# Kernel tuning notes

Hardware: AMD Instinct MI355X
Metric: run time of the kernel (lower is better)

The kernel has to match this reference:

```python
import jax, jax.numpy as jnp
import numpy as np

EPS = 1e-5  # BatchNorm eps (torch default)

def setup_inputs() -> dict:
    key = jax.random.key(0)
    ks = jax.random.split(key, 12)
    B, C, H, W = 4, 256, 64, 64
    IC = 128  # inter_channels = C // 2
    s = 1.0 / np.sqrt(C)
    si = 1.0 / np.sqrt(IC)
    return {
        "x": jax.random.normal(ks[0], (B, C, H, W), jnp.float32),
        "y": jax.random.normal(ks[1], (B, C, H, W), jnp.float32),
        "g_w": jax.random.normal(ks[2], (IC, C), jnp.float32) * s,
        "g_b": jax.random.normal(ks[3], (IC,), jnp.float32) * 0.01,
        "dx_w": jax.random.normal(ks[4], (IC, C), jnp.float32) * s,
        "dx_b": jax.random.normal(ks[5], (IC,), jnp.float32) * 0.01,
        "dy_w": jax.random.normal(ks[6], (IC, C), jnp.float32) * s,
        "dy_b": jax.random.normal(ks[7], (IC,), jnp.float32) * 0.01,
        "w_w": jax.random.normal(ks[8], (C, IC), jnp.float32) * si,
        "w_b": jax.random.normal(ks[9], (C,), jnp.float32) * 0.01,
        "bn_gamma": jax.random.normal(ks[10], (C,), jnp.float32),
        "bn_beta": jax.random.normal(ks[11], (C,), jnp.float32) * 0.01,
    }

def _conv1x1(t, w, b):
    # t: [B,C,H,W], w: [O,C], b: [O] -> [B,O,H,W]
    return jnp.einsum('bchw,oc->bohw', t, w) + b[None, :, None, None]

def reference(x, y, g_w, g_b, dx_w, dx_b, dy_w, dy_b, w_w, w_b, bn_gamma, bn_beta):
    B, C, H, W = x.shape
    IC = g_w.shape[0]
    N = H * W
    g_y = _conv1x1(y, g_w, g_b).reshape(B, IC, N).transpose(0, 2, 1)      # [B,N,IC]
    theta_x = _conv1x1(x, dx_w, dx_b).reshape(B, IC, N).transpose(0, 2, 1)  # [B,N,IC]
    phi_y = _conv1x1(y, dy_w, dy_b).reshape(B, IC, N)                      # [B,IC,N]
    f = jnp.einsum('bnc,bcm->bnm', theta_x, phi_y)                         # [B,N,N]
    f_div_C = jax.nn.softmax(f, axis=-1)
    y2 = jnp.einsum('bnm,bmc->bnc', f_div_C, g_y)                          # [B,N,IC]
    y2 = y2.transpose(0, 2, 1).reshape(B, IC, H, W)
    wy = _conv1x1(y2, w_w, w_b)                                            # [B,C,H,W]
    # BatchNorm2d in training mode: batch stats over (B,H,W) per channel
    mean = jnp.mean(wy, axis=(0, 2, 3), keepdims=True)
    var = jnp.var(wy, axis=(0, 2, 3), keepdims=True)
    wy_bn = (wy - mean) / jnp.sqrt(var + EPS)
    wy_bn = wy_bn * bn_gamma[None, :, None, None] + bn_beta[None, :, None, None]
    return wy_bn + x
```

## Files before the change

### kernel.cpp

```cpp
#include <hip/hip_runtime.h>
#include <hip/hip_bf16.h>
#include <math.h>

typedef unsigned short ushort_t;
typedef __attribute__((ext_vector_type(8))) short     short8;
typedef __attribute__((ext_vector_type(8))) _Float16  half8;
typedef __attribute__((ext_vector_type(8))) unsigned short ushort8;
typedef __attribute__((ext_vector_type(4))) float     float4v;

__device__ __forceinline__ float b2f(ushort_t u) {
    return __uint_as_float(((unsigned)u) << 16);
}
__device__ __forceinline__ ushort_t f2b(float f) {
    unsigned i = __float_as_uint(f);
    return (ushort_t)((i + 0x7FFFu + ((i >> 16) & 1u)) >> 16);
}
__device__ __forceinline__ void split2(float v, ushort_t& h, ushort_t& l) {
    h = f2b(v);
    l = f2b(v - b2f(h));
}
__device__ __forceinline__ void glds16(const ushort_t* g, ushort_t* l) {
    __builtin_amdgcn_global_load_lds((const __attribute__((address_space(1))) void*)g,
                                     (__attribute__((address_space(3))) void*)l, 16, 0, 0);
}

#define WTFH_OFF   0
#define WTFL_OFF   196608
#define WWBH_OFF   393216
#define WWBL_OFF   458752
#define BIAS_OFF   524288
#define STATS_OFF  526336
#define PROJF_OFF  1048576
#define GT_OFF     9437184
#define OPART_OFF  13631488
#define WY_OFF     1048576

__global__ void prep_k(const float* __restrict__ dx_w, const float* __restrict__ dy_w,
                       const float* __restrict__ g_w,  const float* __restrict__ dx_b,
                       const float* __restrict__ dy_b, const float* __restrict__ g_b,
                       const float* __restrict__ w_w,
                       ushort_t* __restrict__ wtfh, ushort_t* __restrict__ wtfl,
                       ushort_t* __restrict__ wwbh, ushort_t* __restrict__ wwbl,
                       float* __restrict__ bias) {
    int idx = blockIdx.x * 256 + threadIdx.x;
    int j = idx & 7, lane = (idx >> 3) & 63, kk = (idx >> 9) & 7, ot = idx >> 12;
    int o = ot * 16 + (lane & 15);
    int c = kk * 32 + ((lane >> 4) * 8) + j;
    float v;
    if (o < 128)      v = dx_w[o * 256 + c];
    else if (o < 256) v = dy_w[(o - 128) * 256 + c];
    else              v = g_w[(o - 256) * 256 + c];
    ushort_t h, l;
    split2(v, h, l);
    wtfh[idx] = h; wtfl[idx] = l;
    if (idx < 32768) {
        split2(w_w[idx], h, l);
        wwbh[idx] = h; wwbl[idx] = l;
    }
    if (idx < 384) {
        bias[idx] = (idx < 128) ? dx_b[idx]
                  : (idx < 256) ? dy_b[idx - 128]
                                : g_b[idx - 256];
    }
}

__global__ __launch_bounds__(256) void proj_k(const float* __restrict__ x,
                                              const float* __restrict__ y,
                                              const ushort_t* __restrict__ wtfh,
                                              const ushort_t* __restrict__ wtfl,
                                              const float* __restrict__ bias,
                                              ushort_t* __restrict__ projf,
                                              ushort_t* __restrict__ gT) {
    __shared__ ushort_t xT[2][32 * 256];
    int b = blockIdx.y, n0 = blockIdx.x * 32;
    int tid = threadIdx.x;
    int w = tid >> 6, lane = tid & 63;
    int mrow = lane & 15, quad = lane >> 4, koff = quad * 8;
    int half = w & 1, sect = w >> 1;
    int arow = half * 16 + mrow;

    for (int s = 0; s < 2; s++) {
        if (s) __syncthreads();
        const float* src = s ? y : x;
        #pragma unroll
        for (int i = 0; i < 4; i++) {
            int ch = tid + i * 256;
            int c = ch >> 2, off = (ch & 3) * 8;
            const float* p = src + (size_t)(b * 256 + c) * 4096 + n0 + off;
            float4v v0 = *(const float4v*)p;
            float4v v1 = *(const float4v*)(p + 4);
            #pragma unroll
            for (int jj = 0; jj < 4; jj++) {
                ushort_t h, l;
                split2(v0[jj], h, l);
                xT[0][(off + jj) * 256 + c] = h;
                xT[1][(off + jj) * 256 + c] = l;
                split2(v1[jj], h, l);
                xT[0][(off + 4 + jj) * 256 + c] = h;
                xT[1][(off + 4 + jj) * 256 + c] = l;
            }
        }
        __syncthreads();

        short8 fh[8], fl[8];
        #pragma unroll
        for (int kk = 0; kk < 8; kk++) {
            fh[kk] = *(const short8*)&xT[0][arow * 256 + kk * 32 + koff];
            fl[kk] = *(const short8*)&xT[1][arow * 256 + kk * 32 + koff];
        }

        int ot0 = s ? (8 + sect * 8) : (sect * 4);
        int ot1 = s ? (ot0 + 8) : (ot0 + 4);
        for (int ot = ot0; ot < ot1; ot++) {
            float4v acc = {0.f, 0.f, 0.f, 0.f};
            #pragma unroll
            for (int kk = 0; kk < 8; kk++) {
                short8 bh = *(const short8*)(wtfh + (size_t)((ot * 8 + kk) * 64 + lane) * 8);
                short8 bl = *(const short8*)(wtfl + (size_t)((ot * 8 + kk) * 64 + lane) * 8);
                acc = __builtin_amdgcn_mfma_f32_16x16x32_bf16(fh[kk], bh, acc, 0, 0, 0);
                acc = __builtin_amdgcn_mfma_f32_16x16x32_bf16(fh[kk], bl, acc, 0, 0, 0);
                acc = __builtin_amdgcn_mfma_f32_16x16x32_bf16(fl[kk], bh, acc, 0, 0, 0);
            }
            int o = ot * 16 + mrow;
            float bo = bias[o];
            #pragma unroll
            for (int r = 0; r < 4; r++) {
                int n = n0 + half * 16 + quad * 4 + r;
                float v = acc[r] + bo;
                if (ot < 16) {
                    _Float16 hf = (_Float16)v;
                    projf[(size_t)(b * 4096 + n) * 256 + o] = *(ushort_t*)&hf;
                } else {
                    gT[(size_t)(b * 128 + (o - 256)) * 4096 + n] = f2b(v);
                }
            }
        }
    }
}

__global__ __launch_bounds__(512, 2) void flash_k(const ushort_t* __restrict__ projf,
                                                  const ushort_t* __restrict__ gT,
                                                  float* __restrict__ opart,
                                                  float* __restrict__ oml,
                                                  int kqlog) {
    __shared__ __align__(16) ushort_t KsF[2][8192];
    __shared__ __align__(16) ushort_t VsF[2][8192];
    __shared__ __align__(16) ushort_t Ps[256 * 72];

    int b = blockIdx.y;
    int kq = blockIdx.x & ((1 << kqlog) - 1);
    int q0 = (blockIdx.x >> kqlog) * 256;
    int iters = 64 >> kqlog;
    int kt0 = kq * iters;
    int tid = threadIdx.x, w = tid >> 6, lane = tid & 63;
    int mrow = lane & 15, quad = lane >> 4, koff = quad * 8;

    int kRow[2], kCol[2], vIc[2], vOf[2], dstB[2];
    #pragma unroll
    for (int i = 0; i < 2; i++) {
        int ck = tid + i * 512, combo = ck >> 6, l2 = ck & 63;
        kRow[i] = (combo >> 2) * 16 + (l2 & 15);
        kCol[i] = 128 + (combo & 3) * 32 + (l2 >> 4) * 8;
        vIc[i]  = (combo >> 1) * 16 + (l2 & 15);
        vOf[i]  = (combo & 1) * 32 + (l2 >> 4) * 8;
        dstB[i] = (i * 512 + w * 64) * 8;
    }

    half8 qf[2][4];
    #pragma unroll
    for (int s = 0; s < 2; s++)
        #pragma unroll
        for (int kk = 0; kk < 4; kk++)
            qf[s][kk] = *(const half8*)(projf + (size_t)(b * 4096 + q0 + w * 32 + s * 16 + mrow) * 256
                                        + kk * 32 + koff);

    float4v oacc[2][8], oaccL[2];
    #pragma unroll
    for (int s = 0; s < 2; s++) {
        oaccL[s] = (float4v){0.f, 0.f, 0.f, 0.f};
        #pragma unroll
        for (int ot = 0; ot < 8; ot++) oacc[s][ot] = (float4v){0.f, 0.f, 0.f, 0.f};
    }
    short8 vones;
    #pragma unroll
    for (int j = 0; j < 8; j++) vones[j] = (short)0x3F80;

    {
        int kb = kt0 * 64;
        #pragma unroll
        for (int i = 0; i < 2; i++) {
            glds16(projf + (size_t)(b * 4096 + kb + kRow[i]) * 256 + kCol[i], &KsF[0][dstB[i]]);
            glds16(gT + (size_t)(b * 128 + vIc[i]) * 4096 + kb + vOf[i], &VsF[0][dstB[i]]);
        }
    }

    for (int kt = kt0; kt < kt0 + iters; kt++) {
        int cur = (kt - kt0) & 1;
        __syncthreads();
        if (kt + 1 < kt0 + iters) {
            int kb = (kt + 1) * 64;
            #pragma unroll
            for (int i = 0; i < 2; i++) {
                glds16(projf + (size_t)(b * 4096 + kb + kRow[i]) * 256 + kCol[i], &KsF[1 - cur][dstB[i]]);
                glds16(gT + (size_t)(b * 128 + vIc[i]) * 4096 + kb + vOf[i], &VsF[1 - cur][dstB[i]]);
            }
        }

        float4v sacc[2][4];
        #pragma unroll
        for (int ct = 0; ct < 4; ct++) {
            float4v a0 = {0.f, 0.f, 0.f, 0.f}, a1 = {0.f, 0.f, 0.f, 0.f};
            #pragma unroll
            for (int kk = 0; kk < 4; kk++) {
                half8 bh = *(const half8*)&KsF[cur][((ct * 4 + kk) * 64 + lane) * 8];
                a0 = __builtin_amdgcn_mfma_f32_16x16x32_f16(qf[0][kk], bh, a0, 0, 0, 0);
                a1 = __builtin_amdgcn_mfma_f32_16x16x32_f16(qf[1][kk], bh, a1, 0, 0, 0);
            }
            sacc[0][ct] = a0; sacc[1][ct] = a1;
        }

        #pragma unroll
        for (int s = 0; s < 2; s++)
            #pragma unroll
            for (int r = 0; r < 4; r++) {
                int prow = w * 32 + s * 16 + quad * 4 + r;
                #pragma unroll
                for (int ct = 0; ct < 4; ct++) {
                    float p = __builtin_exp2f(fmaf(sacc[s][ct][r], 1.44269504f, -92.332481f));
                    Ps[prow * 72 + ct * 16 + mrow] = f2b(p);
                }
            }
        __builtin_amdgcn_s_waitcnt(0xC07F);

        #pragma unroll
        for (int k2 = 0; k2 < 2; k2++) {
            short8 a0 = *(const short8*)&Ps[(w * 32 + mrow) * 72 + k2 * 32 + koff];
            short8 a1 = *(const short8*)&Ps[(w * 32 + 16 + mrow) * 72 + k2 * 32 + koff];
            #pragma unroll
            for (int ot = 0; ot < 8; ot++) {
                short8 bfr = *(const short8*)&VsF[cur][((ot * 2 + k2) * 64 + lane) * 8];
                oacc[0][ot] = __builtin_amdgcn_mfma_f32_16x16x32_bf16(a0, bfr, oacc[0][ot], 0, 0, 0);
                oacc[1][ot] = __builtin_amdgcn_mfma_f32_16x16x32_bf16(a1, bfr, oacc[1][ot], 0, 0, 0);
            }
            oaccL[0] = __builtin_amdgcn_mfma_f32_16x16x32_bf16(a0, vones, oaccL[0], 0, 0, 0);
            oaccL[1] = __builtin_amdgcn_mfma_f32_16x16x32_bf16(a1, vones, oaccL[1], 0, 0, 0);
        }
    }

    #pragma unroll
    for (int s = 0; s < 2; s++)
        #pragma unroll
        for (int ot = 0; ot < 8; ot++)
            #pragma unroll
            for (int r = 0; r < 4; r++) {
                int R = b * 4096 + q0 + w * 32 + s * 16 + quad * 4 + r;
                opart[((size_t)kq * 16384 + R) * 128 + ot * 16 + mrow] = oacc[s][ot][r];
            }
    if (mrow == 0) {
        #pragma unroll
        for (int s = 0; s < 2; s++)
            #pragma unroll
            for (int r = 0; r < 4; r++) {
                int R = b * 4096 + q0 + w * 32 + s * 16 + quad * 4 + r;
                oml[kq * 16384 + R] = oaccL[s][r];
            }
    }
}

__global__ __launch_bounds__(256) void wy_k(const float* __restrict__ opart,
                                            const float* __restrict__ oml,
                                            const ushort_t* __restrict__ wwbh,
                                            const ushort_t* __restrict__ wwbl,
                                            const float* __restrict__ w_b,
                                            ushort_t* __restrict__ wy, int KQ) {
    int b = blockIdx.y, n0 = blockIdx.x * 32;
    int tid = threadIdx.x, w = tid >> 6, lane = tid & 63;
    int mrow = lane & 15, quad = lane >> 4, koff = quad * 8;
    int half = w & 1, sect = w >> 1;
    int Rn = b * 4096 + n0 + half * 16 + mrow;

    float L = 0.f;
    for (int kq = 0; kq < KQ; kq++) L += oml[kq * 16384 + Rn];
    float invL = 1.f / L;

    short8 bfh[4], bfl[4];
    #pragma unroll
    for (int kk = 0; kk < 4; kk++) {
        float a[8];
        #pragma unroll
        for (int j = 0; j < 8; j++) a[j] = 0.f;
        for (int kq = 0; kq < KQ; kq++) {
            const float* p = opart + ((size_t)kq * 16384 + Rn) * 128 + kk * 32 + koff;
            float4v v0 = *(const float4v*)p;
            float4v v1 = *(const float4v*)(p + 4);
            #pragma unroll
            for (int j = 0; j < 4; j++) { a[j] += v0[j]; a[4 + j] += v1[j]; }
        }
        #pragma unroll
        for (int j = 0; j < 8; j++) {
            ushort_t h, l;
            split2(a[j] * invL, h, l);
            bfh[kk][j] = (short)h; bfl[kk][j] = (short)l;
        }
    }

    int coln = n0 + half * 16 + mrow;
    for (int cot = sect * 8; cot < sect * 8 + 8; cot++) {
        float4v acc = {0.f, 0.f, 0.f, 0.f};
        #pragma unroll
        for (int kk = 0; kk < 4; kk++) {
            size_t woff = (size_t)(cot * 16 + mrow) * 128 + kk * 32 + koff;
            short8 ah = *(const short8*)(wwbh + woff);
            short8 al = *(const short8*)(wwbl + woff);
            acc = __builtin_amdgcn_mfma_f32_16x16x32_bf16(ah, bfh[kk], acc, 0, 0, 0);
            acc = __builtin_amdgcn_mfma_f32_16x16x32_bf16(ah, bfl[kk], acc, 0, 0, 0);
            acc = __builtin_amdgcn_mfma_f32_16x16x32_bf16(al, bfh[kk], acc, 0, 0, 0);
        }
        #pragma unroll
        for (int r = 0; r < 4; r++) {
            int co = cot * 16 + quad * 4 + r;
            wy[(size_t)(b * 256 + co) * 4096 + coln] = f2b(acc[r] + w_b[co]);
        }
    }
}

__global__ __launch_bounds__(256) void stats_k(const ushort_t* __restrict__ wy,
                                               float* __restrict__ stats) {
    __shared__ float red[8];
    int co = blockIdx.x, tid = threadIdx.x, w = tid >> 6, lane = tid & 63;
    float s = 0.f, s2 = 0.f;
    #pragma unroll
    for (int i = 0; i < 8; i++) {
        int ch = tid + i * 256;
        int b = ch >> 9, n = (ch & 511) * 8;
        ushort8 v = *(const ushort8*)(wy + (size_t)(b * 256 + co) * 4096 + n);
        #pragma unroll
        for (int j = 0; j < 8; j++) { float f = b2f(v[j]); s += f; s2 += f * f; }
    }
    #pragma unroll
    for (int d = 1; d < 64; d <<= 1) { s += __shfl_xor(s, d, 64); s2 += __shfl_xor(s2, d, 64); }
    if (lane == 0) { red[w] = s; red[4 + w] = s2; }
    __syncthreads();
    if (tid == 0) {
        stats[co]       = red[0] + red[1] + red[2] + red[3];
        stats[256 + co] = red[4] + red[5] + red[6] + red[7];
    }
}

__global__ __launch_bounds__(256) void bn_k(const ushort_t* __restrict__ wy,
                                            const float* __restrict__ x,
                                            const float* __restrict__ gamma,
                                            const float* __restrict__ beta,
                                            const float* __restrict__ stats,
                                            float* __restrict__ out) {
    int idx = (blockIdx.x * 256 + threadIdx.x) * 8;
    int c = (idx >> 12) & 255;
    const float inv_cnt = 1.f / 16384.f;
    float mean = stats[c] * inv_cnt;
    float var  = stats[256 + c] * inv_cnt - mean * mean;
    float inv  = rsqrtf(var + 1e-5f);
    float scale = gamma[c] * inv;
    float shift = beta[c] - mean * scale;
    ushort8 wv = *(const ushort8*)(wy + idx);
    float4v x0 = *(const float4v*)(x + idx);
    float4v x1 = *(const float4v*)(x + idx + 4);
    float4v o0, o1;
    #pragma unroll
    for (int j = 0; j < 4; j++) {
        o0[j] = b2f(wv[j]) * scale + shift + x0[j];
        o1[j] = b2f(wv[4 + j]) * scale + shift + x1[j];
    }
    *(float4v*)(out + idx) = o0;
    *(float4v*)(out + idx + 4) = o1;
}

extern "C" void kernel_launch(void* const* d_in, const int* in_sizes, int n_in,
                              void* d_out, int out_size, void* d_ws, size_t ws_size,
                              hipStream_t stream) {
    const float* x    = (const float*)d_in[0];
    const float* y    = (const float*)d_in[1];
    const float* g_w  = (const float*)d_in[2];
    const float* g_b  = (const float*)d_in[3];
    const float* dx_w = (const float*)d_in[4];
    const float* dx_b = (const float*)d_in[5];
    const float* dy_w = (const float*)d_in[6];
    const float* dy_b = (const float*)d_in[7];
    const float* w_w  = (const float*)d_in[8];
    const float* w_b  = (const float*)d_in[9];
    const float* bn_g = (const float*)d_in[10];
    const float* bn_b = (const float*)d_in[11];

    char* ws = (char*)d_ws;
    ushort_t* wtfh  = (ushort_t*)(ws + WTFH_OFF);
    ushort_t* wtfl  = (ushort_t*)(ws + WTFL_OFF);
    ushort_t* wwbh  = (ushort_t*)(ws + WWBH_OFF);
    ushort_t* wwbl  = (ushort_t*)(ws + WWBL_OFF);
    float*    bias  = (float*)(ws + BIAS_OFF);
    float*    stats = (float*)(ws + STATS_OFF);
    ushort_t* projf = (ushort_t*)(ws + PROJF_OFF);
    ushort_t* gT    = (ushort_t*)(ws + GT_OFF);
    float*    opart = (float*)(ws + OPART_OFF);
    ushort_t* wy    = (ushort_t*)(ws + WY_OFF);
    float*    out   = (float*)d_out;

    int kqlog;
    if      (ws_size >= 13631488u + 4u * (8388608u + 65536u)) kqlog = 2;
    else if (ws_size >= 13631488u + 2u * (8388608u + 65536u)) kqlog = 1;
    else                                                      kqlog = 0;
    int KQ = 1 << kqlog;
    float* oml = (float*)(ws + OPART_OFF + (size_t)KQ * 8388608u);

    prep_k<<<384, 256, 0, stream>>>(dx_w, dy_w, g_w, dx_b, dy_b, g_b, w_w,
                                    wtfh, wtfl, wwbh, wwbl, bias);
    proj_k<<<dim3(128, 4), 256, 0, stream>>>(x, y, wtfh, wtfl, bias, projf, gT);
    flash_k<<<dim3(16 << kqlog, 4), 512, 0, stream>>>(projf, gT, opart, oml, kqlog);
    wy_k<<<dim3(128, 4), 256, 0, stream>>>(opart, oml, wwbh, wwbl, w_b, wy, KQ);
    stats_k<<<256, 256, 0, stream>>>(wy, stats);
    bn_k<<<2048, 256, 0, stream>>>(wy, x, bn_g, bn_b, stats, out);
}
```

Before: 225.6 us.

## Keep softmax probabilities in registers via bpermute, drop LDS P buffer

The flash kernel now computes S^T (K as the A operand) so each lane holds probabilities it can pack to bf16 with v_cvt_pk_bf16_f32 and redistribute into the PV MFMA A-fragment layout via ds_bpermute. This removes the Ps shared-memory round trip and its waitcnt. The row sum is accumulated in registers and reduced with shuffles, replacing the extra ones-vector MFMA. Blocks shrink to 256 threads with 128 query rows each, the grid doubles, and each thread issues twice as many async loads, which trades per-block K/V reuse for lower LDS use and possibly higher occupancy.

```diff
diff --git a/kernel.cpp b/kernel.cpp
--- a/kernel.cpp
+++ b/kernel.cpp
@@ -22,6 +22,11 @@
 __device__ __forceinline__ void glds16(const ushort_t* g, ushort_t* l) {
     __builtin_amdgcn_global_load_lds((const __attribute__((address_space(1))) void*)g,
                                      (__attribute__((address_space(3))) void*)l, 16, 0, 0);
+}
+__device__ __forceinline__ unsigned int pack2bf(float lo, float hi) {
+    unsigned int r;
+    asm("v_cvt_pk_bf16_f32 %0, %1, %2" : "=v"(r) : "v"(lo), "v"(hi));
+    return r;
 }
 
 #define WTFH_OFF   0
@@ -138,33 +143,36 @@
     }
 }
 
-__global__ __launch_bounds__(512, 2) void flash_k(const ushort_t* __restrict__ projf,
+__global__ __launch_bounds__(256, 2) void flash_k(const ushort_t* __restrict__ projf,
                                                   const ushort_t* __restrict__ gT,
                                                   float* __restrict__ opart,
                                                   float* __restrict__ oml,
                                                   int kqlog) {
     __shared__ __align__(16) ushort_t KsF[2][8192];
     __shared__ __align__(16) ushort_t VsF[2][8192];
-    __shared__ __align__(16) ushort_t Ps[256 * 72];
 
     int b = blockIdx.y;
     int kq = blockIdx.x & ((1 << kqlog) - 1);
-    int q0 = (blockIdx.x >> kqlog) * 256;
+    int q0 = (blockIdx.x >> kqlog) * 128;
     int iters = 64 >> kqlog;
     int kt0 = kq * iters;
     int tid = threadIdx.x, w = tid >> 6, lane = tid & 63;
     int mrow = lane & 15, quad = lane >> 4, koff = quad * 8;
 
-    int kRow[2], kCol[2], vIc[2], vOf[2], dstB[2];
-    #pragma unroll
-    for (int i = 0; i < 2; i++) {
-        int ck = tid + i * 512, combo = ck >> 6, l2 = ck & 63;
-        kRow[i] = (combo >> 2) * 16 + (l2 & 15);
-        kCol[i] = 128 + (combo & 3) * 32 + (l2 >> 4) * 8;
-        vIc[i]  = (combo >> 1) * 16 + (l2 & 15);
-        vOf[i]  = (combo & 1) * 32 + (l2 >> 4) * 8;
-        dstB[i] = (i * 512 + w * 64) * 8;
-    }
+    int kRow[4], kCol[4], vIc[4], vOf[4], dstB[4];
+    #pragma unroll
+    for (int i = 0; i < 4; i++) {
+        int c = w + i * 4;
+        kRow[i] = (c >> 2) * 16 + mrow;
+        kCol[i] = 128 + (c & 3) * 32 + koff;
+        vIc[i]  = (c >> 1) * 16 + mrow;
+        vOf[i]  = (c & 1) * 32 + koff;
+        dstB[i] = c * 512;
+    }
+
+    int idx0 = (((quad & 1) << 5) + mrow) << 2;
+    int idx1 = idx0 + 64;
+    bool hiq = quad >= 2;
 
     half8 qf[2][4];
     #pragma unroll
@@ -174,21 +182,17 @@
             qf[s][kk] = *(const half8*)(projf + (size_t)(b * 4096 + q0 + w * 32 + s * 16 + mrow) * 256
                                         + kk * 32 + koff);
 
-    float4v oacc[2][8], oaccL[2];
-    #pragma unroll
-    for (int s = 0; s < 2; s++) {
-        oaccL[s] = (float4v){0.f, 0.f, 0.f, 0.f};
+    float4v oacc[2][8];
+    float lsum[2] = {0.f, 0.f};
+    #pragma unroll
+    for (int s = 0; s < 2; s++)
         #pragma unroll
         for (int ot = 0; ot < 8; ot++) oacc[s][ot] = (float4v){0.f, 0.f, 0.f, 0.f};
-    }
-    short8 vones;
-    #pragma unroll
-    for (int j = 0; j < 8; j++) vones[j] = (short)0x3F80;
 
     {
         int kb = kt0 * 64;
         #pragma unroll
-        for (int i = 0; i < 2; i++) {
+        for (int i = 0; i < 4; i++) {
             glds16(projf + (size_t)(b * 4096 + kb + kRow[i]) * 256 + kCol[i], &KsF[0][dstB[i]]);
             glds16(gT + (size_t)(b * 128 + vIc[i]) * 4096 + kb + vOf[i], &VsF[0][dstB[i]]);
         }
@@ -200,50 +204,64 @@
         if (kt + 1 < kt0 + iters) {
             int kb = (kt + 1) * 64;
             #pragma unroll
-            for (int i = 0; i < 2; i++) {
+            for (int i = 0; i < 4; i++) {
                 glds16(projf + (size_t)(b * 4096 + kb + kRow[i]) * 256 + kCol[i], &KsF[1 - cur][dstB[i]]);
                 glds16(gT + (size_t)(b * 128 + vIc[i]) * 4096 + kb + vOf[i], &VsF[1 - cur][dstB[i]]);
             }
         }
 
-        float4v sacc[2][4];
+        unsigned int pk[2][4][2];
         #pragma unroll
         for (int ct = 0; ct < 4; ct++) {
             float4v a0 = {0.f, 0.f, 0.f, 0.f}, a1 = {0.f, 0.f, 0.f, 0.f};
             #pragma unroll
             for (int kk = 0; kk < 4; kk++) {
-                half8 bh = *(const half8*)&KsF[cur][((ct * 4 + kk) * 64 + lane) * 8];
-                a0 = __builtin_amdgcn_mfma_f32_16x16x32_f16(qf[0][kk], bh, a0, 0, 0, 0);
-                a1 = __builtin_amdgcn_mfma_f32_16x16x32_f16(qf[1][kk], bh, a1, 0, 0, 0);
-            }
-            sacc[0][ct] = a0; sacc[1][ct] = a1;
-        }
-
-        #pragma unroll
-        for (int s = 0; s < 2; s++)
+                half8 ah = *(const half8*)&KsF[cur][((ct * 4 + kk) * 64 + lane) * 8];
+                a0 = __builtin_amdgcn_mfma_f32_16x16x32_f16(ah, qf[0][kk], a0, 0, 0, 0);
+                a1 = __builtin_amdgcn_mfma_f32_16x16x32_f16(ah, qf[1][kk], a1, 0, 0, 0);
+            }
+            float p0[4], p1[4];
             #pragma unroll
             for (int r = 0; r < 4; r++) {
-                int prow = w * 32 + s * 16 + quad * 4 + r;
-                #pragma unroll
-                for (int ct = 0; ct < 4; ct++) {
-                    float p = __builtin_exp2f(fmaf(sacc[s][ct][r], 1.44269504f, -92.332481f));
-                    Ps[prow * 72 + ct * 16 + mrow] = f2b(p);
-                }
-            }
-        __builtin_amdgcn_s_waitcnt(0xC07F);
+                p0[r] = __builtin_exp2f(fmaf(a0[r], 1.44269504f, -92.332481f));
+                p1[r] = __builtin_exp2f(fmaf(a1[r], 1.44269504f, -92.332481f));
+            }
+            lsum[0] += (p0[0] + p0[1]) + (p0[2] + p0[3]);
+            lsum[1] += (p1[0] + p1[1]) + (p1[2] + p1[3]);
+            pk[0][ct][0] = pack2bf(p0[0], p0[1]);
+            pk[0][ct][1] = pack2bf(p0[2], p0[3]);
+            pk[1][ct][0] = pack2bf(p1[0], p1[1]);
+            pk[1][ct][1] = pack2bf(p1[2], p1[3]);
+        }
 
         #pragma unroll
         for (int k2 = 0; k2 < 2; k2++) {
-            short8 a0 = *(const short8*)&Ps[(w * 32 + mrow) * 72 + k2 * 32 + koff];
-            short8 a1 = *(const short8*)&Ps[(w * 32 + 16 + mrow) * 72 + k2 * 32 + koff];
+            short8 af[2];
+            #pragma unroll
+            for (int s = 0; s < 2; s++) {
+                int A0 = (int)pk[s][2 * k2][0],     A1 = (int)pk[s][2 * k2][1];
+                int B0 = (int)pk[s][2 * k2 + 1][0], B1 = (int)pk[s][2 * k2 + 1][1];
+                int gA0l = __builtin_amdgcn_ds_bpermute(idx0, A0);
+                int gA1l = __builtin_amdgcn_ds_bpermute(idx0, A1);
+                int gB0l = __builtin_amdgcn_ds_bpermute(idx0, B0);
+                int gB1l = __builtin_amdgcn_ds_bpermute(idx0, B1);
+                int gA0h = __builtin_amdgcn_ds_bpermute(idx1, A0);
+                int gA1h = __builtin_amdgcn_ds_bpermute(idx1, A1);
+                int gB0h = __builtin_amdgcn_ds_bpermute(idx1, B0);
+                int gB1h = __builtin_amdgcn_ds_bpermute(idx1, B1);
+                union { int u[4]; short8 s8; } fu;
+                fu.u[0] = hiq ? gB0l : gA0l;
+                fu.u[1] = hiq ? gB1l : gA1l;
+                fu.u[2] = hiq ? gB0h : gA0h;
+                fu.u[3] = hiq ? gB1h : gA1h;
+                af[s] = fu.s8;
+            }
             #pragma unroll
             for (int ot = 0; ot < 8; ot++) {
                 short8 bfr = *(const short8*)&VsF[cur][((ot * 2 + k2) * 64 + lane) * 8];
-                oacc[0][ot] = __builtin_amdgcn_mfma_f32_16x16x32_bf16(a0, bfr, oacc[0][ot], 0, 0, 0);
-                oacc[1][ot] = __builtin_amdgcn_mfma_f32_16x16x32_bf16(a1, bfr, oacc[1][ot], 0, 0, 0);
-            }
-            oaccL[0] = __builtin_amdgcn_mfma_f32_16x16x32_bf16(a0, vones, oaccL[0], 0, 0, 0);
-            oaccL[1] = __builtin_amdgcn_mfma_f32_16x16x32_bf16(a1, vones, oaccL[1], 0, 0, 0);
+                oacc[0][ot] = __builtin_amdgcn_mfma_f32_16x16x32_bf16(af[0], bfr, oacc[0][ot], 0, 0, 0);
+                oacc[1][ot] = __builtin_amdgcn_mfma_f32_16x16x32_bf16(af[1], bfr, oacc[1][ot], 0, 0, 0);
+            }
         }
     }
 
@@ -256,14 +274,13 @@
                 int R = b * 4096 + q0 + w * 32 + s * 16 + quad * 4 + r;
                 opart[((size_t)kq * 16384 + R) * 128 + ot * 16 + mrow] = oacc[s][ot][r];
             }
-    if (mrow == 0) {
-        #pragma unroll
-        for (int s = 0; s < 2; s++)
-            #pragma unroll
-            for (int r = 0; r < 4; r++) {
-                int R = b * 4096 + q0 + w * 32 + s * 16 + quad * 4 + r;
-                oml[kq * 16384 + R] = oaccL[s][r];
-            }
+    #pragma unroll
+    for (int s = 0; s < 2; s++) {
+        float l = lsum[s];
+        l += __shfl_xor(l, 16, 64);
+        l += __shfl_xor(l, 32, 64);
+        if (lane < 16)
+            oml[kq * 16384 + b * 4096 + q0 + w * 32 + s * 16 + lane] = l;
     }
 }
 
@@ -413,7 +430,7 @@
     prep_k<<<384, 256, 0, stream>>>(dx_w, dy_w, g_w, dx_b, dy_b, g_b, w_w,
                                     wtfh, wtfl, wwbh, wwbl, bias);
     proj_k<<<dim3(128, 4), 256, 0, stream>>>(x, y, wtfh, wtfl, bias, projf, gT);
-    flash_k<<<dim3(16 << kqlog, 4), 512, 0, stream>>>(projf, gT, opart, oml, kqlog);
+    flash_k<<<dim3(32 << kqlog, 4), 256, 0, stream>>>(projf, gT, opart, oml, kqlog);
     wy_k<<<dim3(128, 4), 256, 0, stream>>>(opart, oml, wwbh, wwbl, w_b, wy, KQ);
     stats_k<<<256, 256, 0, stream>>>(wy, stats);
     bn_k<<<2048, 256, 0, stream>>>(wy, x, bn_g, bn_b, stats, out);
```

After: 218.4 us. 3.2% less time.
